# Kernel tuning notes

Hardware: AMD Instinct MI355X
Metric: run time of the kernel (lower is better)

Reference implementation:

```python
import jax, jax.numpy as jnp
import numpy as np

B, T, H, M, S, E, IN = 8, 2048, 64, 32, 20, 3, 32
EPS = 1e-8  # torch CosineSimilarity eps


def setup_inputs() -> dict:
    key = jax.random.key(0)
    ks = jax.random.split(key, 7)
    return {
        "x": jax.random.normal(ks[0], (B, T, IN), jnp.float32),
        "hidden": jax.random.normal(ks[1], (E, B, T, H), jnp.float32),
        "memory": jax.random.normal(ks[2], (S, M), jnp.float32),
        "Wq": jax.random.normal(ks[3], (E, H, M), jnp.float32),
        "Wk": jax.random.normal(ks[4], (E, H, M), jnp.float32),
        "Wv": jax.random.normal(ks[5], (E, H, M), jnp.float32),
        "input_query": jax.random.normal(ks[6], (IN, M), jnp.float32),
    }


def _cosine(a, b):
    # torch.nn.CosineSimilarity(dim=-1): each vector norm clamped to eps
    na = jnp.maximum(jnp.linalg.norm(a, axis=-1), EPS)
    nb = jnp.maximum(jnp.linalg.norm(b, axis=-1), EPS)
    return jnp.sum(a * b, axis=-1) / (na * nb)


def reference(x, hidden, memory, Wq, Wk, Wv, input_query):
    # query_mem: soft read from global memory slots
    q_in = jnp.einsum('bti,im->btm', x, input_query)           # [B,T,M]
    mem_sc = jax.nn.softmax(jnp.einsum('btm,sm->bts', q_in, memory), axis=-1)
    memories = jnp.einsum('bts,sm->btm', mem_sc, memory)       # [B,T,M]

    # per-expert tiny self-attention (vectorized over expert axis e)
    Q = jnp.einsum('ebth,ehm->ebtm', hidden, Wq)
    K = jnp.einsum('ebth,ehm->ebtm', hidden, Wk)
    V = jnp.einsum('ebth,ehm->ebtm', hidden, Wv)
    energy = jnp.einsum('ebtm,ebsm->ebts', Q, K)               # [E,B,T,T]
    att = jax.nn.softmax(energy, axis=-1)
    out = jnp.einsum('ebts,ebsm->ebtm', att, V)                # [E,B,T,M]

    cos = _cosine(memories[None], out)                         # [E,B,T]
    return jnp.moveaxis(cos, 0, -1)                            # [B,T,E]
```

## Files before the change

kernel.cpp:

```cpp
#include <hip/hip_runtime.h>
#include <hip/hip_bf16.h>

#define Bv  8
#define Tv  2048
#define Hv  64
#define Mv  32
#define Sv  20
#define Ev  3
#define INv 32
#define LOG2E 1.44269504088896340736f

typedef __attribute__((ext_vector_type(8))) _Float16 half8;
typedef __attribute__((ext_vector_type(4))) _Float16 half4v;
typedef __attribute__((ext_vector_type(2))) __fp16 fp16x2;
typedef __attribute__((ext_vector_type(4))) float float4v;

__global__ __launch_bounds__(256) void qkv_kernel(
    const float* __restrict__ hidden,
    const float* __restrict__ Wq,
    const float* __restrict__ Wk,
    const float* __restrict__ Wv,
    const float* __restrict__ x,
    const float* __restrict__ memory,
    const float* __restrict__ iq,
    _Float16* __restrict__ Qh, _Float16* __restrict__ Ql,
    _Float16* __restrict__ Kh, _Float16* __restrict__ Kl,
    _Float16* __restrict__ Vth,
    float* __restrict__ memout)
{
    __shared__ __align__(16) char sBlob[24576];
    __shared__ float sIQ[32][32];
    __shared__ float sM[20][32];

    int bid  = blockIdx.x;
    int tile = bid & 31;
    int b    = (bid >> 5) & 7;
    int e    = bid >> 8;
    int tid  = threadIdx.x;
    int lane = tid & 63;
    int w    = tid >> 6;
    int quad = lane >> 4;
    int l15  = lane & 15;
    size_t eb = (size_t)(e * Bv + b);
    size_t row0 = eb * Tv + (size_t)tile * 64;
    const float* hbase = hidden + row0 * Hv;

    const float* arow = hbase + (size_t)(w * 16 + l15) * Hv + quad * 8;
    float4 a0 = *(const float4*)(arow);
    float4 a1 = *(const float4*)(arow + 4);
    float4 a2 = *(const float4*)(arow + 32);
    float4 a3 = *(const float4*)(arow + 36);

    if (e == 0) {
        for (int i = tid; i < 32 * 32; i += 256) sIQ[i >> 5][i & 31] = iq[i];
        for (int i = tid; i < 20 * 32; i += 256) sM[i >> 5][i & 31] = memory[i];
    }

    {
        const float* wsrc[3] = {Wq + (size_t)e * Hv * Mv,
                                Wk + (size_t)e * Hv * Mv,
                                Wv + (size_t)e * Hv * Mv};
#pragma unroll
        for (int j = 0; j < 3; ++j) {
            int u  = tid + j * 256;
            int c  = u >> 3, kb = u & 7;
            const float* src = wsrc[c >> 5] + (c & 31);
            float scale = (c < 32) ? LOG2E : 1.f;
            half8 hi, lo;
#pragma unroll
            for (int i = 0; i < 8; ++i) {
                float v = src[(kb * 8 + i) * Mv] * scale;
                _Float16 hh = (_Float16)v;
                hi[i] = hh;
                lo[i] = (_Float16)(v - (float)hh);
            }
            int off = c * 128 + ((kb ^ (c & 7)) << 4);
            *(half8*)(sBlob + off)         = hi;
            *(half8*)(sBlob + 12288 + off) = lo;
        }
    }

    half8 aH0, aL0, aH1, aL1;
    {
        float vv[8] = {a0.x, a0.y, a0.z, a0.w, a1.x, a1.y, a1.z, a1.w};
#pragma unroll
        for (int i = 0; i < 8; ++i) {
            _Float16 hh = (_Float16)vv[i];
            aH0[i] = hh; aL0[i] = (_Float16)(vv[i] - (float)hh);
        }
        float ww[8] = {a2.x, a2.y, a2.z, a2.w, a3.x, a3.y, a3.z, a3.w};
#pragma unroll
        for (int i = 0; i < 8; ++i) {
            _Float16 hh = (_Float16)ww[i];
            aH1[i] = hh; aL1[i] = (_Float16)(ww[i] - (float)hh);
        }
    }

    __syncthreads();

    float4v accs[6];
    int x7 = l15 & 7;
#pragma unroll
    for (int ct = 0; ct < 6; ++ct) {
        const char* brow = sBlob + (ct * 16 + l15) * 128;
        half8 bH0 = *(const half8*)(brow + ((quad ^ x7) << 4));
        half8 bH1 = *(const half8*)(brow + (((4 + quad) ^ x7) << 4));
        half8 bL0 = *(const half8*)(brow + 12288 + ((quad ^ x7) << 4));
        half8 bL1 = *(const half8*)(brow + 12288 + (((4 + quad) ^ x7) << 4));
        float4v acc = {0.f, 0.f, 0.f, 0.f};
        acc = __builtin_amdgcn_mfma_f32_16x16x32_f16(aH0, bL0, acc, 0, 0, 0);
        acc = __builtin_amdgcn_mfma_f32_16x16x32_f16(aL0, bH0, acc, 0, 0, 0);
        acc = __builtin_amdgcn_mfma_f32_16x16x32_f16(aH0, bH0, acc, 0, 0, 0);
        acc = __builtin_amdgcn_mfma_f32_16x16x32_f16(aH1, bL1, acc, 0, 0, 0);
        acc = __builtin_amdgcn_mfma_f32_16x16x32_f16(aL1, bH1, acc, 0, 0, 0);
        acc = __builtin_amdgcn_mfma_f32_16x16x32_f16(aH1, bH1, acc, 0, 0, 0);
        accs[ct] = acc;
    }

    __syncthreads();

    char* sQh = sBlob;
    char* sQl = sBlob + 4096;
    char* sKh = sBlob + 8192;
    char* sKl = sBlob + 12288;
    char* sVh = sBlob + 16384;
    int rbase = w * 16 + quad * 4;
#pragma unroll
    for (int ct = 0; ct < 6; ++ct) {
        int c = ct * 16 + l15;
#pragma unroll
        for (int r = 0; r < 4; ++r) {
            int row = rbase + r;
            float v = accs[ct][r];
            if (ct < 2) {
                _Float16 h16 = (_Float16)v;
                *(_Float16*)(sQh + row * 64 + c * 2) = h16;
                *(_Float16*)(sQl + row * 64 + c * 2) = (_Float16)(v - (float)h16);
            } else if (ct < 4) {
                _Float16 h16 = (_Float16)v;
                int m = c - 32;
                int off = row * 64 + m * 2;
                *(_Float16*)(sKh + off) = h16;
                *(_Float16*)(sKl + off) = (_Float16)(v - (float)h16);
            } else {
                int d = c - 64;
                int off = d * 128 + row * 2;
                *(_Float16*)(sVh + off) = (_Float16)v;
            }
        }
    }
    __syncthreads();

    size_t pb = eb * (size_t)Tv * 32 + (size_t)tile * 2048;
    _Float16* dsts[5] = {Qh + pb, Ql + pb, Kh + pb, Kl + pb, Vth + pb};
#pragma unroll
    for (int pl = 0; pl < 5; ++pl)
        ((float4*)dsts[pl])[tid] = ((const float4*)(sBlob + pl * 4096))[tid];

    if (e == 0 && tid < 64) {
        int t = b * Tv + tile * 64 + tid;
        const float4* xr = (const float4*)(x + (size_t)t * INv);
        float xv[32];
#pragma unroll
        for (int i = 0; i < 8; ++i) {
            float4 v = xr[i];
            xv[4*i] = v.x; xv[4*i+1] = v.y; xv[4*i+2] = v.z; xv[4*i+3] = v.w;
        }
        float qm[32];
#pragma unroll
        for (int m = 0; m < 32; ++m) qm[m] = 0.f;
        for (int i = 0; i < 32; ++i) {
            float xi = xv[i];
#pragma unroll
            for (int m4 = 0; m4 < 8; ++m4) {
                float4 wv = *(const float4*)&sIQ[i][m4 * 4];
                qm[4*m4]   = fmaf(xi, wv.x, qm[4*m4]);
                qm[4*m4+1] = fmaf(xi, wv.y, qm[4*m4+1]);
                qm[4*m4+2] = fmaf(xi, wv.z, qm[4*m4+2]);
                qm[4*m4+3] = fmaf(xi, wv.w, qm[4*m4+3]);
            }
        }
        float sc[20];
#pragma unroll
        for (int j = 0; j < 20; ++j) {
            float a2 = 0.f;
#pragma unroll
            for (int m = 0; m < 32; ++m) a2 = fmaf(qm[m], sM[j][m], a2);
            sc[j] = a2;
        }
        float mx = sc[0];
#pragma unroll
        for (int j = 1; j < 20; ++j) mx = fmaxf(mx, sc[j]);
        float psum = 0.f, p[20];
#pragma unroll
        for (int j = 0; j < 20; ++j) { p[j] = exp2f((sc[j] - mx) * LOG2E); psum += p[j]; }
        float inv = 1.0f / psum;
        float mo[32];
#pragma unroll
        for (int m = 0; m < 32; ++m) mo[m] = 0.f;
        for (int j = 0; j < 20; ++j) {
            float pj = p[j];
#pragma unroll
            for (int m = 0; m < 32; ++m) mo[m] = fmaf(pj, sM[j][m], mo[m]);
        }
        float4* outp = (float4*)(memout + (size_t)t * Mv);
#pragma unroll
        for (int m4 = 0; m4 < 8; ++m4) {
            float4 v;
            v.x = mo[4*m4] * inv; v.y = mo[4*m4+1] * inv;
            v.z = mo[4*m4+2] * inv; v.w = mo[4*m4+3] * inv;
            outp[m4] = v;
        }
    }
}

#define ATT_LOAD(c, KH, KL, V0, V1)                                           \
    {                                                                         \
        size_t ko = ebOff + (size_t)((c) * 64 + w * 16 + l15) * 32 + quad * 8;\
        KH = *(const half8*)(Kh + ko);                                        \
        KL = *(const half8*)(Kl + ko);                                        \
        size_t vo = ebOff + (size_t)(c) * 2048 + (size_t)l15 * 64             \
                    + w * 16 + quad * 4;                                      \
        V0 = *(const half4v*)(Vth + vo);                                      \
        V1 = *(const half4v*)(Vth + vo + 1024);                               \
    }

#define ATT_BODY(KH, KL, V0, V1)                                              \
    _Pragma("unroll")                                                         \
    for (int qt = 0; qt < 4; ++qt) {                                          \
        float4v acc = {0.f, 0.f, 0.f, 0.f};                                   \
        acc = __builtin_amdgcn_mfma_f32_16x16x32_f16(KH, qL[qt], acc, 0,0,0); \
        acc = __builtin_amdgcn_mfma_f32_16x16x32_f16(KL, qH[qt], acc, 0,0,0); \
        acc = __builtin_amdgcn_mfma_f32_16x16x32_f16(KH, qH[qt], acc, 0,0,0); \
        float pmax = fmaxf(fmaxf(acc[0], acc[1]), fmaxf(acc[2], acc[3]));     \
        pmax = fmaxf(pmax, __shfl_xor(pmax, 16));                             \
        pmax = fmaxf(pmax, __shfl_xor(pmax, 32));                             \
        if (__any(pmax > mm[qt] + 8.0f)) {                                    \
            float mn = fmaxf(mm[qt], pmax);                                   \
            float al = exp2f(mm[qt] - mn);                                    \
            mm[qt] = mn;                                                      \
            _Pragma("unroll")                                                 \
            for (int r = 0; r < 4; ++r) {                                     \
                O[qt][0][r] *= al; O[qt][1][r] *= al;                         \
            }                                                                 \
        }                                                                     \
        fp16x2 p01 = __builtin_amdgcn_cvt_pkrtz(exp2f(acc[0] - mm[qt]),       \
                                                exp2f(acc[1] - mm[qt]));      \
        fp16x2 p23 = __builtin_amdgcn_cvt_pkrtz(exp2f(acc[2] - mm[qt]),       \
                                                exp2f(acc[3] - mm[qt]));      \
        unsigned long long up =                                               \
            ((unsigned long long)__builtin_bit_cast(unsigned int, p23) << 32) \
            | __builtin_bit_cast(unsigned int, p01);                          \
        half4v pB = __builtin_bit_cast(half4v, up);                           \
        O[qt][0] = __builtin_amdgcn_mfma_f32_16x16x16f16(V0, pB, O[qt][0],    \
                                                         0, 0, 0);            \
        O[qt][1] = __builtin_amdgcn_mfma_f32_16x16x16f16(V1, pB, O[qt][1],    \
                                                         0, 0, 0);            \
    }

__global__ __launch_bounds__(256, 3) void attn_kernel(
    const _Float16* __restrict__ Qh, const _Float16* __restrict__ Ql,
    const _Float16* __restrict__ Kh, const _Float16* __restrict__ Kl,
    const _Float16* __restrict__ Vth,
    const float* __restrict__ memv,
    float* __restrict__ out)
{
    __shared__ float sO[4][64][33];
    __shared__ float sMw[4][64];

    int bid  = blockIdx.x;
    int xcd  = bid & 7;
    int slot = bid >> 3;
    int tile = slot & 31;
    int ebi  = xcd + ((slot >> 5) << 3);
    int e    = ebi >> 3;
    int b    = ebi & 7;
    int tid  = threadIdx.x;
    int lane = tid & 63;
    int w    = tid >> 6;
    int quad = lane >> 4;
    int l15  = lane & 15;
    size_t eb = (size_t)ebi;
    size_t ebOff = eb * (size_t)Tv * 32;

    half8 qH[4], qL[4];
#pragma unroll
    for (int qt = 0; qt < 4; ++qt) {
        size_t qoff = ebOff + (size_t)(tile * 64 + qt * 16 + l15) * 32 + quad * 8;
        qH[qt] = *(const half8*)(Qh + qoff);
        qL[qt] = *(const half8*)(Ql + qoff);
    }

    float4v O[4][2];
#pragma unroll
    for (int qt = 0; qt < 4; ++qt) {
        O[qt][0] = {0.f, 0.f, 0.f, 0.f};
        O[qt][1] = {0.f, 0.f, 0.f, 0.f};
    }
    float mm[4] = {-3.0e38f, -3.0e38f, -3.0e38f, -3.0e38f};

    half8 kHa, kLa, kHb, kLb;
    half4v v0a, v1a, v0b, v1b;
    ATT_LOAD(0, kHa, kLa, v0a, v1a);

    for (int c = 0; c < 32; c += 2) {
        ATT_LOAD(c + 1, kHb, kLb, v0b, v1b);
        ATT_BODY(kHa, kLa, v0a, v1a);
        if (c + 2 < 32) ATT_LOAD(c + 2, kHa, kLa, v0a, v1a);
        ATT_BODY(kHb, kLb, v0b, v1b);
    }

#pragma unroll
    for (int qt = 0; qt < 4; ++qt) {
        int q = qt * 16 + l15;
        sMw[w][q] = mm[qt];
#pragma unroll
        for (int dh = 0; dh < 2; ++dh)
#pragma unroll
            for (int r = 0; r < 4; ++r)
                sO[w][q][dh * 16 + quad * 4 + r] = O[qt][dh][r];
    }
    __syncthreads();

    int q  = tid >> 2;
    int dq = tid & 3;
    float ms0 = sMw[0][q], ms1 = sMw[1][q], ms2 = sMw[2][q], ms3 = sMw[3][q];
    float M  = fmaxf(fmaxf(ms0, ms1), fmaxf(ms2, ms3));
    float g0 = exp2f(ms0 - M), g1 = exp2f(ms1 - M);
    float g2 = exp2f(ms2 - M), g3 = exp2f(ms3 - M);
    const float* mb = memv + ((size_t)b * Tv + tile * 64 + q) * 32 + dq * 8;
    float dotm = 0.f, oo = 0.f, mm2 = 0.f;
#pragma unroll
    for (int j = 0; j < 8; ++j) {
        int d = dq * 8 + j;
        float o = g0 * sO[0][q][d] + g1 * sO[1][q][d]
                + g2 * sO[2][q][d] + g3 * sO[3][q][d];
        float mvv = mb[j];
        dotm = fmaf(o, mvv, dotm);
        oo   = fmaf(o, o, oo);
        mm2  = fmaf(mvv, mvv, mm2);
    }
    dotm += __shfl_xor(dotm, 1); dotm += __shfl_xor(dotm, 2);
    oo   += __shfl_xor(oo, 1);   oo   += __shfl_xor(oo, 2);
    mm2  += __shfl_xor(mm2, 1);  mm2  += __shfl_xor(mm2, 2);
    if (dq == 0) {
        float na = fmaxf(sqrtf(mm2), 1e-8f);
        float nb = fmaxf(sqrtf(oo), 1e-30f);
        out[((size_t)b * Tv + tile * 64 + q) * Ev + e] = dotm / (na * nb);
    }
}

extern "C" void kernel_launch(void* const* d_in, const int* in_sizes, int n_in,
                              void* d_out, int out_size, void* d_ws, size_t ws_size,
                              hipStream_t stream) {
    const float* x      = (const float*)d_in[0];
    const float* hidden = (const float*)d_in[1];
    const float* memory = (const float*)d_in[2];
    const float* Wq     = (const float*)d_in[3];
    const float* Wk     = (const float*)d_in[4];
    const float* Wv     = (const float*)d_in[5];
    const float* iq     = (const float*)d_in[6];
    float* out          = (float*)d_out;

    char* ws = (char*)d_ws;
    const size_t PLANE = (size_t)Ev * Bv * Tv * 32 * 2;
    float*    memout = (float*)ws;
    _Float16* Qh  = (_Float16*)(ws + 2097152);
    _Float16* Ql  = (_Float16*)(ws + 2097152 + PLANE);
    _Float16* Kh  = (_Float16*)(ws + 2097152 + 2 * PLANE);
    _Float16* Kl  = (_Float16*)(ws + 2097152 + 3 * PLANE);
    _Float16* Vth = (_Float16*)(ws + 2097152 + 4 * PLANE);

    qkv_kernel<<<Ev * Bv * (Tv / 64), 256, 0, stream>>>(hidden, Wq, Wk, Wv,
                                                        x, memory, iq,
                                                        Qh, Ql, Kh, Kl, Vth, memout);
    attn_kernel<<<Ev * Bv * (Tv / 64), 256, 0, stream>>>(Qh, Ql, Kh, Kl, Vth,
                                                         memout, out);
}
```

Before: 147.5 us.

## Skip negligible attention tiles, coalesce weight loads, spread memory-read over threads

The attention loop now checks each 16-key tile's per-lane score max and skips the exp and PV MFMAs when every score is more than 20 (log2 units) below the running max. The cross-lane max shuffles now run only when a rescale is needed. The QKV kernel loads weights as contiguous float4 rows instead of strided scalars, and the memory soft-read spreads each token over 4 threads with shuffle reductions instead of 64 threads doing full 32-wide loops. The skip drops contributions below about 2^-20 of the row max, which is a small approximation that pays off most when softmax rows are sharply peaked.

```diff
diff --git a/kernel.cpp b/kernel.cpp
--- a/kernel.cpp
+++ b/kernel.cpp
@@ -60,23 +60,25 @@
         const float* wsrc[3] = {Wq + (size_t)e * Hv * Mv,
                                 Wk + (size_t)e * Hv * Mv,
                                 Wv + (size_t)e * Hv * Mv};
-#pragma unroll
-        for (int j = 0; j < 3; ++j) {
-            int u  = tid + j * 256;
-            int c  = u >> 3, kb = u & 7;
-            const float* src = wsrc[c >> 5] + (c & 31);
-            float scale = (c < 32) ? LOG2E : 1.f;
-            half8 hi, lo;
-#pragma unroll
-            for (int i = 0; i < 8; ++i) {
-                float v = src[(kb * 8 + i) * Mv] * scale;
+        int h  = tid >> 2;
+        int m0 = (tid & 3) * 8;
+        int kb = h >> 3, wi = h & 7;
+#pragma unroll
+        for (int p = 0; p < 3; ++p) {
+            const float4* src = (const float4*)(wsrc[p] + (size_t)tid * 8);
+            float4 wa = src[0], wb = src[1];
+            float wv8[8] = {wa.x, wa.y, wa.z, wa.w, wb.x, wb.y, wb.z, wb.w};
+            float scale = (p == 0) ? LOG2E : 1.f;
+#pragma unroll
+            for (int j = 0; j < 8; ++j) {
+                int c = p * 32 + m0 + j;
+                float v = wv8[j] * scale;
                 _Float16 hh = (_Float16)v;
-                hi[i] = hh;
-                lo[i] = (_Float16)(v - (float)hh);
+                _Float16 ll = (_Float16)(v - (float)hh);
+                int off = c * 128 + ((kb ^ (c & 7)) << 4) + wi * 2;
+                *(_Float16*)(sBlob + off)         = hh;
+                *(_Float16*)(sBlob + 12288 + off) = ll;
             }
-            int off = c * 128 + ((kb ^ (c & 7)) << 4);
-            *(half8*)(sBlob + off)         = hi;
-            *(half8*)(sBlob + 12288 + off) = lo;
         }
     }
 
@@ -157,35 +159,39 @@
     for (int pl = 0; pl < 5; ++pl)
         ((float4*)dsts[pl])[tid] = ((const float4*)(sBlob + pl * 4096))[tid];
 
-    if (e == 0 && tid < 64) {
-        int t = b * Tv + tile * 64 + tid;
+    if (e == 0) {
+        int tok4 = tid >> 2;
+        int m0   = (tid & 3) * 8;
+        int t = b * Tv + tile * 64 + tok4;
         const float4* xr = (const float4*)(x + (size_t)t * INv);
-        float xv[32];
-#pragma unroll
-        for (int i = 0; i < 8; ++i) {
-            float4 v = xr[i];
-            xv[4*i] = v.x; xv[4*i+1] = v.y; xv[4*i+2] = v.z; xv[4*i+3] = v.w;
-        }
-        float qm[32];
-#pragma unroll
-        for (int m = 0; m < 32; ++m) qm[m] = 0.f;
-        for (int i = 0; i < 32; ++i) {
-            float xi = xv[i];
-#pragma unroll
-            for (int m4 = 0; m4 < 8; ++m4) {
-                float4 wv = *(const float4*)&sIQ[i][m4 * 4];
-                qm[4*m4]   = fmaf(xi, wv.x, qm[4*m4]);
-                qm[4*m4+1] = fmaf(xi, wv.y, qm[4*m4+1]);
-                qm[4*m4+2] = fmaf(xi, wv.z, qm[4*m4+2]);
-                qm[4*m4+3] = fmaf(xi, wv.w, qm[4*m4+3]);
+        float qm[8];
+#pragma unroll
+        for (int m = 0; m < 8; ++m) qm[m] = 0.f;
+#pragma unroll
+        for (int i4 = 0; i4 < 8; ++i4) {
+            float4 xv = xr[i4];
+            float xs[4] = {xv.x, xv.y, xv.z, xv.w};
+#pragma unroll
+            for (int s = 0; s < 4; ++s) {
+                int i = i4 * 4 + s;
+                float xi = xs[s];
+                float4 w0 = *(const float4*)&sIQ[i][m0];
+                float4 w1 = *(const float4*)&sIQ[i][m0 + 4];
+                qm[0] = fmaf(xi, w0.x, qm[0]); qm[1] = fmaf(xi, w0.y, qm[1]);
+                qm[2] = fmaf(xi, w0.z, qm[2]); qm[3] = fmaf(xi, w0.w, qm[3]);
+                qm[4] = fmaf(xi, w1.x, qm[4]); qm[5] = fmaf(xi, w1.y, qm[5]);
+                qm[6] = fmaf(xi, w1.z, qm[6]); qm[7] = fmaf(xi, w1.w, qm[7]);
             }
         }
         float sc[20];
 #pragma unroll
         for (int j = 0; j < 20; ++j) {
-            float a2 = 0.f;
-#pragma unroll
-            for (int m = 0; m < 32; ++m) a2 = fmaf(qm[m], sM[j][m], a2);
+            float4 s0 = *(const float4*)&sM[j][m0];
+            float4 s1 = *(const float4*)&sM[j][m0 + 4];
+            float a2 = qm[0] * s0.x + qm[1] * s0.y + qm[2] * s0.z + qm[3] * s0.w
+                     + qm[4] * s1.x + qm[5] * s1.y + qm[6] * s1.z + qm[7] * s1.w;
+            a2 += __shfl_xor(a2, 1);
+            a2 += __shfl_xor(a2, 2);
             sc[j] = a2;
         }
         float mx = sc[0];
@@ -195,22 +201,24 @@
 #pragma unroll
         for (int j = 0; j < 20; ++j) { p[j] = exp2f((sc[j] - mx) * LOG2E); psum += p[j]; }
         float inv = 1.0f / psum;
-        float mo[32];
-#pragma unroll
-        for (int m = 0; m < 32; ++m) mo[m] = 0.f;
+        float mo[8];
+#pragma unroll
+        for (int m = 0; m < 8; ++m) mo[m] = 0.f;
+#pragma unroll
         for (int j = 0; j < 20; ++j) {
             float pj = p[j];
-#pragma unroll
-            for (int m = 0; m < 32; ++m) mo[m] = fmaf(pj, sM[j][m], mo[m]);
-        }
-        float4* outp = (float4*)(memout + (size_t)t * Mv);
-#pragma unroll
-        for (int m4 = 0; m4 < 8; ++m4) {
-            float4 v;
-            v.x = mo[4*m4] * inv; v.y = mo[4*m4+1] * inv;
-            v.z = mo[4*m4+2] * inv; v.w = mo[4*m4+3] * inv;
-            outp[m4] = v;
-        }
+            float4 s0 = *(const float4*)&sM[j][m0];
+            float4 s1 = *(const float4*)&sM[j][m0 + 4];
+            mo[0] = fmaf(pj, s0.x, mo[0]); mo[1] = fmaf(pj, s0.y, mo[1]);
+            mo[2] = fmaf(pj, s0.z, mo[2]); mo[3] = fmaf(pj, s0.w, mo[3]);
+            mo[4] = fmaf(pj, s1.x, mo[4]); mo[5] = fmaf(pj, s1.y, mo[5]);
+            mo[6] = fmaf(pj, s1.z, mo[6]); mo[7] = fmaf(pj, s1.w, mo[7]);
+        }
+        float4* outp = (float4*)(memout + (size_t)t * Mv + m0);
+        float4 o0 = {mo[0] * inv, mo[1] * inv, mo[2] * inv, mo[3] * inv};
+        float4 o1 = {mo[4] * inv, mo[5] * inv, mo[6] * inv, mo[7] * inv};
+        outp[0] = o0;
+        outp[1] = o1;
     }
 }
 
@@ -232,11 +240,12 @@
         acc = __builtin_amdgcn_mfma_f32_16x16x32_f16(KH, qL[qt], acc, 0,0,0); \
         acc = __builtin_amdgcn_mfma_f32_16x16x32_f16(KL, qH[qt], acc, 0,0,0); \
         acc = __builtin_amdgcn_mfma_f32_16x16x32_f16(KH, qH[qt], acc, 0,0,0); \
-        float pmax = fmaxf(fmaxf(acc[0], acc[1]), fmaxf(acc[2], acc[3]));     \
-        pmax = fmaxf(pmax, __shfl_xor(pmax, 16));                             \
-        pmax = fmaxf(pmax, __shfl_xor(pmax, 32));                             \
-        if (__any(pmax > mm[qt] + 8.0f)) {                                    \
-            float mn = fmaxf(mm[qt], pmax);                                   \
+        float pmax4 = fmaxf(fmaxf(acc[0], acc[1]), fmaxf(acc[2], acc[3]));    \
+        if (!__any(pmax4 > mm[qt] - 20.0f)) continue;    \
+        if (__any(pmax4 > mm[qt] + 8.0f)) {                 \
+            float pm = fmaxf(pmax4, __shfl_xor(pmax4, 16));                   \
+            pm = fmaxf(pm, __shfl_xor(pm, 32));                               \
+            float mn = fmaxf(mm[qt], pm);                                     \
             float al = exp2f(mm[qt] - mn);                                    \
             mm[qt] = mn;                                                      \
             _Pragma("unroll")                                                 \
```

After: 135.8 us. 8.0% less time.
